# Kernel tuning notes

Measured on AMD Instinct MI355X. Metric: run time of the kernel, lower is better.

The kernel has to match this reference:

```python
import jax, jax.numpy as jnp
import numpy as np
from jax.scipy.special import xlogy

LAMBDA_XM = 0.05
LAMBDA_SEG2D = 1.0
BN_EPS = 1e-5


def setup_inputs() -> dict:
    key = jax.random.key(0)
    ks = jax.random.split(key, 40)
    S, N, Nv, B, Np, M, H, C, MID = 2, 240000, 80000, 2, 120000, 30000, 64, 20, 16
    Nimg = B * M
    f = lambda i, shape, s=0.05: jax.random.normal(ks[i], shape, jnp.float32) * s
    inp = {
        'img_feat': f(0, (S, Nimg, H), 1.0),
        'pts_feat': f(1, (S, Nv, H), 1.0),
        'coors_inv': jax.random.randint(ks[2], (S, N), 0, Nv),
        'labels': jax.random.randint(ks[3], (N,), 0, C),
        'img_label': jax.random.randint(ks[4], (Nimg,), 0, C),
        'p2img_idx': jax.random.randint(ks[5], (B, M), 0, Np),
        # multihead 3d classifiers (per scale): Linear(H,128)-ReLU-Linear(128,C)
        'w3a': f(6, (S, H, 128)), 'b3a': jnp.zeros((S, 128)),
        'w3b': f(7, (S, 128, C)), 'b3b': jnp.zeros((S, C)),
        # multihead fuse classifiers
        'wfa': f(8, (S, H, 128)), 'bfa': jnp.zeros((S, 128)),
        'wfb': f(9, (S, 128, C)), 'bfb': jnp.zeros((S, C)),
        # attention: fc1(H->H//4), fc2(H->H//4), fc3(H//2->2), conv1/conv2 (1x1 -> linear) + BN
        'fc1w': f(10, (S, H, MID)), 'fc1b': jnp.zeros((S, MID)),
        'fc2w': f(11, (S, H, MID)), 'fc2b': jnp.zeros((S, MID)),
        'fc3w': f(12, (S, 2 * MID, 2)), 'fc3b': jnp.zeros((S, 2)),
        'c1w': f(13, (S, H, H)), 'c1b': jnp.zeros((S, H)),
        'bn1g': jnp.ones((S, H)), 'bn1b': jnp.zeros((S, H)),
        'c2w': f(14, (S, H, H)), 'c2b': jnp.zeros((S, H)),
        'bn2g': jnp.ones((S, H)), 'bn2b': jnp.zeros((S, H)),
        # final classifier Linear(S*H,128)-ReLU-Linear(128,C)
        'clw1': f(15, (S * H, 128)), 'clb1': jnp.zeros((128,)),
        'clw2': f(16, (128, C)), 'clb2': jnp.zeros((C,)),
    }
    return inp


def _mlp2(x, w1, b1, w2, b2):
    return jax.nn.relu(x @ w1 + b1) @ w2 + b2


def _ce(logits, lab):
    logp = jax.nn.log_softmax(logits, -1)
    return -jnp.take_along_axis(logp, lab[:, None], axis=1).mean()


def _lovasz(probs, lab):
    # lovasz-softmax over all classes, averaged over present classes
    C = probs.shape[1]
    fg = jax.nn.one_hot(lab, C, dtype=probs.dtype)  # [N,C]
    errors = jnp.abs(fg - probs)

    def per_class(err_c, fg_c):
        order = jnp.argsort(-err_c)
        e = err_c[order]
        f = fg_c[order]
        gts = f.sum()
        inter = gts - jnp.cumsum(f)
        union = gts + jnp.cumsum(1.0 - f)
        jac = 1.0 - inter / union
        jac = jnp.concatenate([jac[:1], jac[1:] - jac[:-1]])
        return jnp.dot(e, jac)

    losses = jax.vmap(per_class)(errors.T, fg.T)  # [C]
    present = (fg.sum(0) > 0).astype(probs.dtype)
    return jnp.sum(losses * present) / jnp.maximum(present.sum(), 1.0)


def _seg_loss(logits, lab):
    return _ce(logits, lab) + _lovasz(jax.nn.softmax(logits, -1), lab)


def _convbn_relu(x, cw, cb, g, b):
    # 1x1 Conv1d == per-point linear; BN (training-mode batch stats over points)
    y = x @ cw + cb
    mu = y.mean(0)
    var = y.var(0)
    return jax.nn.relu((y - mu) * jax.lax.rsqrt(var + BN_EPS) * g + b)


def reference(img_feat, pts_feat, coors_inv, labels, img_label, p2img_idx,
              w3a, b3a, w3b, b3b, wfa, bfa, wfb, bfb,
              fc1w, fc1b, fc2w, fc2b, fc3w, fc3b,
              c1w, c1b, bn1g, bn1b, c2w, c2b, bn2g, bn2b,
              clw1, clb1, clw2, clb2):
    S, Nv, H = pts_feat.shape
    C = w3b.shape[-1]
    B, M = p2img_idx.shape
    N = labels.shape[0]
    Np = N // B
    # p2img_mapping: per-batch gather composed to one global gather (batch blocks are contiguous/equal)
    gidx = (jnp.arange(B)[:, None] * Np + p2img_idx).reshape(-1)  # [Nimg]

    loss = jnp.float32(0.0)
    feats = []
    for s in range(S):
        pred3d = _mlp2(pts_feat[s], w3a[s], b3a[s], w3b[s], b3b[s])  # [Nv,C]
        # voxelize_labels: majority vote per voxel (== unique+scatter_max count argmax)
        counts = jnp.zeros((Nv, C), jnp.float32).at[coors_inv[s], labels].add(1.0)
        vox_lab = jnp.argmax(counts, axis=1)  # [Nv]
        # gather voxel feats/preds to image-projected points (fused gather)
        idx = coors_inv[s][gidx]  # [Nimg]
        p = pts_feat[s][idx]      # [Nimg,H] pseudo feats
        pts_pred = pred3d[idx]    # [Nimg,C]
        v = img_feat[s]           # [Nimg,H] valid (image) feats
        # Attention fusion
        w = jax.nn.sigmoid(
            jnp.concatenate([p @ fc1w[s] + fc1b[s], v @ fc2w[s] + fc2b[s]], -1) @ fc3w[s] + fc3b[s])  # [Nimg,2]
        fuse = (_convbn_relu(p, c1w[s], c1b[s], bn1g[s], bn1b[s]) * w[:, 0:1]
                + _convbn_relu(v, c2w[s], c2b[s], bn2g[s], bn2b[s]) * w[:, 1:2])
        feats.append(fuse)
        fuse_pred = _mlp2(fuse, wfa[s], bfa[s], wfb[s], bfb[s])
        loss = loss + _seg_loss(pred3d, vox_lab)
        loss = loss + _seg_loss(fuse_pred, img_label) * LAMBDA_SEG2D / S
        # F.kl_div(log_softmax(pts_pred), softmax(fuse_pred)), reduction='mean' over all elements
        pf = jax.nn.softmax(fuse_pred, -1)
        kl = jnp.mean(xlogy(pf, pf) - pf * jax.nn.log_softmax(pts_pred, -1))
        loss = loss + kl * LAMBDA_XM / S
    img_logits = _mlp2(jnp.concatenate(feats, -1), clw1, clb1, clw2, clb2)
    loss = loss + _seg_loss(img_logits, img_label)
    return loss
```

## Files before the change

### kernel.cpp

```cpp
#include <hip/hip_runtime.h>
#include <stdint.h>

static constexpr int NV   = 80000;
static constexpr int NPT  = 240000;
static constexpr int NIMG = 60000;
static constexpr int Hh   = 64;
static constexpr int Cc   = 20;
static constexpr int NPp  = 120000;
static constexpr int Mm   = 30000;
static constexpr int NB     = 8192;
static constexpr int NCH    = 16;
static constexpr int NBLK_GA  = (NIMG + 63) / 64;
static constexpr int NBLK_MLP = NV / 64;
static constexpr int NBLK_CNT = (NPT + 255) / 256;
static constexpr int NBLK_FILL_NV = (NV + 255) / 256;
static constexpr int NBLK_FILL_NI = (NIMG + 255) / 256;
static constexpr int NBLK_HIST = Cc * NCH;
#define BN_EPS 1e-5f

using bf16x8 = __attribute__((ext_vector_type(8))) short;
using f32x4  = __attribute__((ext_vector_type(4))) float;

__device__ __forceinline__ float waveReduce(float v) {
  #pragma unroll
  for (int o = 32; o > 0; o >>= 1) v += __shfl_down(v, o);
  return v;
}
__device__ __forceinline__ short f2bf(float f) {
  uint32_t u = __float_as_uint(f);
  return (short)((u + 0x7FFFu + ((u >> 16) & 1u)) >> 16);
}
__device__ __forceinline__ float bf2f(uint32_t h) { return __uint_as_float(h << 16); }
__device__ __forceinline__ uint32_t pk2(float a, float b) {
  return ((uint32_t)(uint16_t)f2bf(a)) | ((uint32_t)(uint16_t)f2bf(b) << 16);
}

struct PackDesc { const float* src; short* dst; int K, Nr, nt; };
struct PackArgs { PackDesc d[14]; };

__global__ void __launch_bounds__(256)
k_pack_zero(PackArgs pa,
            const float* __restrict__ fc1w, const float* __restrict__ fc1b,
            const float* __restrict__ fc2w, const float* __restrict__ fc2b,
            const float* __restrict__ fc3w, const float* __restrict__ fc3b,
            float* __restrict__ attEffs,
            uint4* __restrict__ zb, int zq) {
  if (blockIdx.x >= 128) {
    const uint4 z = make_uint4(0u, 0u, 0u, 0u);
    int i = (blockIdx.x - 128) * 256 + threadIdx.x;
    for (; i < zq; i += 256 * 256) zb[i] = z;
    return;
  }
  const int stride = 128 * 256;
  for (int di = 0; di < 14; di++) {
    const float* src = pa.d[di].src;
    short* dst = pa.d[di].dst;
    int K = pa.d[di].K, Nr = pa.d[di].Nr, ntiles = pa.d[di].nt;
    int total = (K / 32) * ntiles * 512;
    for (int idx = blockIdx.x * blockDim.x + threadIdx.x; idx < total; idx += stride) {
      int j = idx & 7, lane = (idx >> 3) & 63, tile = idx >> 9;
      int nt = tile % ntiles, kt = tile / ntiles;
      int k = kt * 32 + (lane >> 4) * 8 + j;
      int n = nt * 16 + (lane & 15);
      float v = (n < Nr) ? src[(size_t)k * Nr + n] : 0.f;
      dst[idx] = f2bf(v);
    }
  }
  if (blockIdx.x < 2 && threadIdx.x < 64) {
    int s = blockIdx.x, t = threadIdx.x;
    const float* f1w = fc1w + s * 64 * 16; const float* f1b = fc1b + s * 16;
    const float* f2w = fc2w + s * 64 * 16; const float* f2b = fc2b + s * 16;
    const float* f3w = fc3w + s * 64;      const float* f3b = fc3b + s * 2;
    float* aE = attEffs + s * 320;
    float p0 = 0.f, p1 = 0.f, v0 = 0.f, v1 = 0.f;
    #pragma unroll
    for (int j = 0; j < 16; j++) {
      p0 = fmaf(f1w[t * 16 + j], f3w[j * 2], p0);
      p1 = fmaf(f1w[t * 16 + j], f3w[j * 2 + 1], p1);
      v0 = fmaf(f2w[t * 16 + j], f3w[(16 + j) * 2], v0);
      v1 = fmaf(f2w[t * 16 + j], f3w[(16 + j) * 2 + 1], v1);
    }
    aE[t * 2] = p0; aE[t * 2 + 1] = p1;
    aE[128 + t * 2] = v0; aE[128 + t * 2 + 1] = v1;
    if (t == 0) {
      float b0 = f3b[0], b1 = f3b[1];
      for (int j = 0; j < 16; j++) {
        b0 += f1b[j] * f3w[j * 2] + f2b[j] * f3w[(16 + j) * 2];
        b1 += f1b[j] * f3w[j * 2 + 1] + f2b[j] * f3w[(16 + j) * 2 + 1];
      }
      aE[256] = b0; aE[257] = b1;
    }
  }
}

__device__ void scanbin_body(const uint32_t* __restrict__ Hb, const uint32_t* __restrict__ HFb,
                             int n, int call, float* __restrict__ lossesC5,
                             int* __restrict__ gts5, int cls) {
  __shared__ int sWC[4], sWF[4];
  __shared__ float sRedF[4];
  int t = threadIdx.x;
  int lane = t & 63, w = t >> 6;
  const uint32_t* Hc  = Hb  + (size_t)cls * NB;
  const uint32_t* HFc = HFb + (size_t)cls * NB;
  int locC = 0, locF = 0;
  #pragma unroll
  for (int i = 0; i < 8; i++) {
    uint4 cv = *(const uint4*)(Hc  + t * 32 + i * 4);
    uint4 fv = *(const uint4*)(HFc + t * 32 + i * 4);
    locC += (int)(cv.x + cv.y + cv.z + cv.w);
    locF += (int)(fv.x + fv.y + fv.z + fv.w);
  }
  int sc = locC, sf = locF;
  #pragma unroll
  for (int o = 1; o < 64; o <<= 1) {
    int a = __shfl_up(sc, o);
    int b = __shfl_up(sf, o);
    if (lane >= o) { sc += a; sf += b; }
  }
  if (lane == 63) { sWC[w] = sc; sWF[w] = sf; }
  __syncthreads();
  int offC = 0, offF = 0, Ftot = 0;
  #pragma unroll
  for (int ww = 0; ww < 4; ww++) {
    int fc = sWF[ww];
    Ftot += fc;
    if (ww < w) { offC += sWC[ww]; offF += fc; }
  }
  int runC = offC + sc - locC;
  int runF = offF + sf - locF;
  float gts = (float)Ftot;
  float contrib = 0.f;
  #pragma unroll
  for (int i = 0; i < 8; i++) {
    uint4 cv = *(const uint4*)(Hc  + t * 32 + i * 4);
    uint4 fv = *(const uint4*)(HFc + t * 32 + i * 4);
    uint32_t ca[4] = {cv.x, cv.y, cv.z, cv.w};
    uint32_t fa[4] = {fv.x, fv.y, fv.z, fv.w};
    #pragma unroll
    for (int j = 0; j < 4; j++) {
      int cnt = (int)ca[j], fgc = (int)fa[j];
      runC += cnt; runF += fgc;
      if (cnt > 0 && Ftot > 0) {
        float r0 = (float)(n - runC);
        float F0 = (float)(Ftot - runF);
        float r1 = r0 + (float)cnt;
        float F1 = F0 + (float)fgc;
        float emean = __uint_as_float((uint32_t)(t * 32 + i * 4 + j) << 17);
        contrib += emean * (r1 / (gts + r1 - F1) - r0 / (gts + r0 - F0));
      }
    }
  }
  contrib = waveReduce(contrib);
// ... 15 lines not shown
  constexpr int KT1 = D / 32;
  const int t = threadIdx.x;
  const int lane = t & 63, w = t >> 6;
  const int m = lane & 15, quad = lane >> 4;
  const int rowA = 16 * w + m;
  bf16x8 a1[KT1];
  #pragma unroll
  for (int kt = 0; kt < KT1; kt++)
    a1[kt] = *(const bf16x8*)(sXb + rowA * LDB + kt * 32 + quad * 8);
  const bf16x8* b1 = (const bf16x8*)pw1;
  #pragma unroll
  for (int nt = 0; nt < 8; nt++) {
    f32x4 c = {0.f, 0.f, 0.f, 0.f};
    #pragma unroll
    for (int kt = 0; kt < KT1; kt++)
      c = __builtin_amdgcn_mfma_f32_16x16x32_bf16(a1[kt], b1[(kt * 8 + nt) * 64 + lane], c, 0, 0, 0);
    int col = nt * 16 + m;
    float bc = B1[col];
    #pragma unroll
    for (int reg = 0; reg < 4; reg++)
      sH[(16 * w + quad * 4 + reg) * 136 + col] = f2bf(fmaxf(c[reg] + bc, 0.f));
  }
  __syncthreads();
  bf16x8 a2[4];
  #pragma unroll
  for (int kt = 0; kt < 4; kt++)
    a2[kt] = *(const bf16x8*)(sH + rowA * 136 + kt * 32 + quad * 8);
  const bf16x8* b2 = (const bf16x8*)pw2;
  #pragma unroll
  for (int nt = 0; nt < 2; nt++) {
    f32x4 c = {0.f, 0.f, 0.f, 0.f};
    #pragma unroll
    for (int kt = 0; kt < 4; kt++)
      c = __builtin_amdgcn_mfma_f32_16x16x32_bf16(a2[kt], b2[(kt * 2 + nt) * 64 + lane], c, 0, 0, 0);
    int col = nt * 16 + m;
    if (col < Cc) {
      float bc = B2[col];
      #pragma unroll
      for (int reg = 0; reg < 4; reg++) {
        int gr = r0 + 16 * w + quad * 4 + reg;
        if (gr < rows) Out[(size_t)gr * Cc + col] = c[reg] + bc;
      }
    }
  }
}

__device__ void mlp64_body(int bid0, const float* __restrict__ X,
    const short* __restrict__ pw1, const float* __restrict__ B1,
    const short* __restrict__ pw2, const float* __restrict__ B2,
    float* __restrict__ Out, int rows, char* smem) {
  short* sXb = (short*)smem;
  short* sH  = (short*)(smem + 9216);
  int t = threadIdx.x, r0 = bid0 * 64;
  for (int i = t; i < 1024; i += 256) {
    int r = i >> 4, k4 = (i & 15) * 4;
    int gr = r0 + r;
    float4 v = (gr < rows) ? *(const float4*)(X + (size_t)gr * 64 + k4)
                           : make_float4(0.f, 0.f, 0.f, 0.f);
    uint2 p; p.x = pk2(v.x, v.y); p.y = pk2(v.z, v.w);
    *(uint2*)(sXb + r * 72 + k4) = p;
  }
  __syncthreads();
  mfma_mlp_body<64>(sXb, sH, r0, rows, pw1, B1, pw2, B2, Out);
}

__device__ void mlp128_body(int bid0, const uint16_t* __restrict__ Xh,
    const short* __restrict__ pw1, const float* __restrict__ B1,
    const short* __restrict__ pw2, const float* __restrict__ B2,
    float* __restrict__ Out, char* smem) {
  short* sXb = (short*)smem;
  short* sH  = (short*)(smem + 17408);
  int t = threadIdx.x, r0 = bid0 * 64;
  for (int i = t; i < 2048; i += 256) {
    int r = i >> 5, k4 = (i & 31) * 4;
    int gr = r0 + r;
    uint2 p = (gr < NIMG) ? *(const uint2*)(Xh + (size_t)gr * 128 + k4) : make_uint2(0u, 0u);
    *(uint2*)(sXb + r * 136 + k4) = p;
  }
  __syncthreads();
  mfma_mlp_body<128>(sXb, sH, r0, NIMG, pw1, B1, pw2, B2, Out);
}

__device__ void cnt_body(int bid0, const int* __restrict__ ci, const int* __restrict__ labels,
                         int* __restrict__ counts, const int* __restrict__ p2img,
                         int* __restrict__ idx) {
  int i = bid0 * 256 + threadIdx.x;
  if (i < NIMG) {
    int b = (i >= Mm) ? 1 : 0;
    idx[i] = ci[b * NPp + p2img[i]];
  }
  if (i < NPT) atomicAdd(&counts[(size_t)ci[i] * Cc + labels[i]], 1);
}

__device__ void colred_body(int bid0, const float* __restrict__ partials,
                            float* __restrict__ red64) {
  int t = threadIdx.x, j = bid0;
  float v = 0.f;
  for (int b = j; b < NBLK_GA; b += 64) v += partials[(size_t)b * 256 + t];
  red64[j * 256 + t] = v;
}

__device__ void fill_body(int bid0, const float* __restrict__ logits,
                          const int* __restrict__ lab, const int* __restrict__ vcnt,
                          int n, uint16_t* __restrict__ E,
                          float ceScale, float* __restrict__ lossAcc,
                          const float* __restrict__ pred3d, const int* __restrict__ idxg,
                          float klScale) {
  int i = bid0 * 256 + threadIdx.x;
  float total = 0.f;
  if (i < n) {
    int lb;
    if (vcnt) {
      const int* crow = vcnt + (size_t)i * Cc;
      int best = crow[0], arg = 0;
      #pragma unroll
      for (int k = 1; k < Cc; k++) {
        int ck = crow[k];
        if (ck > best) { best = ck; arg = k; }
      }
      lb = arg;
    } else {
      lb = lab[i];
    }
    const float* l = logits + (size_t)i * Cc;
    float m = l[0];
    #pragma unroll
    for (int c = 1; c < Cc; c++) m = fmaxf(m, l[c]);
    float ex[Cc]; float se = 0.f;
    #pragma unroll
    for (int c = 0; c < Cc; c++) { ex[c] = expf(l[c] - m); se += ex[c]; }
    float inv = 1.f / se;
    float lse = logf(se);
    total = -(l[lb] - m - lse) * ceScale;
    #pragma unroll
    for (int c = 0; c < Cc; c++) {
      float prob = ex[c] * inv;
      int fg = (c == lb) ? 1 : 0;
      float err = fg ? (1.f - prob) : prob;
      err = fmaxf(err, 0.f);
      uint32_t key = __float_as_uint(err) >> 17;
      E[(size_t)c * n + i] = (uint16_t)((key << 1) | (uint32_t)fg);
    }
    if (pred3d) {
      const float* q = pred3d + (size_t)idxg[i] * Cc;
      float mq = q[0];
      #pragma unroll
      for (int c = 1; c < Cc; c++) mq = fmaxf(mq, q[c]);
      float sq = 0.f;
      #pragma unroll
      for (int c = 0; c < Cc; c++) sq += expf(q[c] - mq);
      float lsq = logf(sq);
      float kl = 0.f;
      #pragma unroll
      for (int c = 0; c < Cc; c++) {
        float lf = l[c] - m - lse;
        float pf = ex[c] * inv;
        float lq = q[c] - mq - lsq;
        kl += pf * (lf - lq);
      }
      total += kl * klScale;
    }
  }
  total = waveReduce(total);
  __shared__ float sh[4];
  int lane = threadIdx.x & 63, w = threadIdx.x >> 6;
  if (lane == 0) sh[w] = total;
  __syncthreads();
  if (threadIdx.x == 0) atomicAdd(lossAcc, sh[0] + sh[1] + sh[2] + sh[3]);
}

__device__ void hist_body(int bid0, const uint16_t* __restrict__ E, int n,
                          uint32_t* __restrict__ H, uint32_t* __restrict__ HF, char* smem) {
  uint32_t* lcf = (uint32_t*)smem;
// ... 122 lines not shown
  }
  __syncthreads();
  {
    int kind = t >> 6, col = t & 63;
    int nt = col >> 4, mm = col & 15;
    float v = 0.f;
    #pragma unroll
    for (int ww = 0; ww < 4; ww++)
      v += sStat[(ww * 4 + nt) * 64 + kind * 16 + mm];
    partials[(size_t)bid0 * 256 + kind * 64 + col] = v;
  }
  if (t < 64) {
    int gr = r0 + t;
    if (gr < NIMG) {
      float l0 = attEff[256] + sAtt[t * 8] + sAtt[t * 8 + 2] + sAtt[t * 8 + 4] + sAtt[t * 8 + 6];
      float l1 = attEff[257] + sAtt[t * 8 + 1] + sAtt[t * 8 + 3] + sAtt[t * 8 + 5] + sAtt[t * 8 + 7];
      attw[gr * 2]     = 1.f / (1.f + expf(-l0));
      attw[gr * 2 + 1] = 1.f / (1.f + expf(-l1));
    }
  }
}

__device__ void fusemlp_body(int bid0,
    const uint16_t* __restrict__ y1, const uint16_t* __restrict__ y2,
    const float* __restrict__ attw, const float* __restrict__ red64,
    const float* __restrict__ g1, const float* __restrict__ be1,
    const float* __restrict__ g2, const float* __restrict__ be2,
    uint16_t* __restrict__ feats, int s64,
    const short* __restrict__ pw1, const float* __restrict__ B1,
    const short* __restrict__ pw2, const float* __restrict__ B2,
    float* __restrict__ Out, char* smem) {
  short* sXb = (short*)smem;
  short* sH  = (short*)(smem + 9216);
  float* sBn = (float*)(smem + 9216 + 17408);
  int t = threadIdx.x, r0 = bid0 * 64;
  float acc = 0.f;
  #pragma unroll 8
  for (int b = 0; b < 64; b++) acc += red64[b * 256 + t];
  float* sSum = (float*)sH;
  sSum[t] = acc;
  __syncthreads();
  if (t < 64) {
    float nn = (float)NIMG;
    float mu1 = sSum[t] / nn;
    float var1 = sSum[64 + t] / nn - mu1 * mu1;
    float a1 = g1[t] / sqrtf(var1 + BN_EPS);
    sBn[t] = a1; sBn[64 + t] = be1[t] - mu1 * a1;
    float mu2 = sSum[128 + t] / nn;
    float var2 = sSum[192 + t] / nn - mu2 * mu2;
    float a2 = g2[t] / sqrtf(var2 + BN_EPS);
    sBn[128 + t] = a2; sBn[192 + t] = be2[t] - mu2 * a2;
  }
  __syncthreads();
  for (int i = t; i < 1024; i += 256) {
    int r = i >> 4, q = i & 15;
    int gr = r0 + r;
    uint2 zp = make_uint2(0u, 0u);
    if (gr < NIMG) {
      float4 a1 = *(const float4*)(sBn + q * 4);
      float4 c1 = *(const float4*)(sBn + 64 + q * 4);
      float4 a2 = *(const float4*)(sBn + 128 + q * 4);
      float4 c2 = *(const float4*)(sBn + 192 + q * 4);
      uint2 u1 = *(const uint2*)(y1 + (size_t)gr * 64 + q * 4);
      uint2 u2 = *(const uint2*)(y2 + (size_t)gr * 64 + q * 4);
      float w0 = attw[gr * 2], w1 = attw[gr * 2 + 1];
      float zx = fmaxf(fmaf(bf2f(u1.x & 0xffff), a1.x, c1.x), 0.f) * w0
               + fmaxf(fmaf(bf2f(u2.x & 0xffff), a2.x, c2.x), 0.f) * w1;
      float zy = fmaxf(fmaf(bf2f(u1.x >> 16),   a1.y, c1.y), 0.f) * w0
               + fmaxf(fmaf(bf2f(u2.x >> 16),   a2.y, c2.y), 0.f) * w1;
      float zz = fmaxf(fmaf(bf2f(u1.y & 0xffff), a1.z, c1.z), 0.f) * w0
               + fmaxf(fmaf(bf2f(u2.y & 0xffff), a2.z, c2.z), 0.f) * w1;
      float zw = fmaxf(fmaf(bf2f(u1.y >> 16),   a1.w, c1.w), 0.f) * w0
               + fmaxf(fmaf(bf2f(u2.y >> 16),   a2.w, c2.w), 0.f) * w1;
      zp.x = pk2(zx, zy); zp.y = pk2(zz, zw);
      *(uint2*)(feats + (size_t)gr * 128 + s64 + q * 4) = zp;
    }
    *(uint2*)(sXb + r * 72 + q * 4) = zp;
  }
  __syncthreads();
  mfma_mlp_body<64>(sXb, sH, r0, NIMG, pw1, B1, pw2, B2, Out);
}

__global__ void __launch_bounds__(256)
k_start2(const float* __restrict__ X0, const float* __restrict__ X1,
         const short* pw1_0, const float* B1_0, const short* pw2_0, const float* B2_0, float* out0,
         const short* pw1_1, const float* B1_1, const short* pw2_1, const float* B2_1, float* out1,
         const int* __restrict__ ci0, const int* __restrict__ ci1,
         const int* __restrict__ labels, const int* __restrict__ p2img,
         int* __restrict__ counts0, int* __restrict__ counts1,
         int* __restrict__ idx0, int* __restrict__ idx1) {
  __shared__ char smem[26624];
  int bid = blockIdx.x;
  if (bid < NBLK_MLP) { mlp64_body(bid, X0, pw1_0, B1_0, pw2_0, B2_0, out0, NV, smem); return; }
  bid -= NBLK_MLP;
  if (bid < NBLK_MLP) { mlp64_body(bid, X1, pw1_1, B1_1, pw2_1, B2_1, out1, NV, smem); return; }
  bid -= NBLK_MLP;
  if (bid < NBLK_CNT) { cnt_body(bid, ci0, labels, counts0, p2img, idx0); return; }
  cnt_body(bid - NBLK_CNT, ci1, labels, counts1, p2img, idx1);
}

__global__ void __launch_bounds__(256)
k_fill2(const float* __restrict__ l0, const int* __restrict__ vc0, uint16_t* __restrict__ E0,
        const float* __restrict__ l1, const int* __restrict__ vc1, uint16_t* __restrict__ E1,
        float ce, float* __restrict__ lossAcc) {
  if (blockIdx.x < NBLK_FILL_NV)
    fill_body(blockIdx.x, l0, nullptr, vc0, NV, E0, ce, lossAcc, nullptr, nullptr, 0.f);
  else
    fill_body(blockIdx.x - NBLK_FILL_NV, l1, nullptr, vc1, NV, E1, ce, lossAcc, nullptr, nullptr, 0.f);
}

__global__ void __launch_bounds__(256)
k_hist2x(const uint16_t* __restrict__ E0, uint32_t* H0, uint32_t* HF0,
         const uint16_t* __restrict__ E1, uint32_t* H1, uint32_t* HF1, int n) {
  __shared__ char smem[32768];
  if (blockIdx.x < NBLK_HIST) hist_body(blockIdx.x, E0, n, H0, HF0, smem);
  else hist_body(blockIdx.x - NBLK_HIST, E1, n, H1, HF1, smem);
}

__global__ void __launch_bounds__(256)
k_gattx(const float* __restrict__ pts, const int* __restrict__ idx, const float* __restrict__ img,
        const short* pc1, const float* c1b, const short* pc2, const float* c2b,
        const float* attEff, uint16_t* y1, uint16_t* y2, float* attw, float* partials,
        const uint32_t* Ha, const uint32_t* HFa, int na, int calla,
        const uint32_t* Hb, const uint32_t* HFb, int nb, int callb,
        int nscan,
        const float* crPart, float* crRed,
        float* lossesC5, int* gts5) {
  __shared__ char smem[24576];
  int bid = blockIdx.x;
  if (bid < nscan * Cc) {
    if (bid < Cc) scanbin_body(Ha, HFa, na, calla, lossesC5, gts5, bid);
    else scanbin_body(Hb, HFb, nb, callb, lossesC5, gts5, bid - Cc);
    return;
  }
  bid -= nscan * Cc;
  if (crPart) {
    if (bid < 64) { colred_body(bid, crPart, crRed); return; }
    bid -= 64;
  }
  gatt_body(bid, pts, idx, img, pc1, c1b, pc2, c2b, attEff, y1, y2, attw, partials, smem);
}

__global__ void __launch_bounds__(256)
k_fusex(const uint16_t* y1, const uint16_t* y2, const float* attw, const float* red64,
        const float* g1, const float* be1, const float* g2, const float* be2,
        uint16_t* feats, int s64,
        const short* pw1, const float* B1, const short* pw2, const float* B2, float* Out,
        const float* crPart, float* crRed,
        const float* fl_logits, const int* fl_lab, uint16_t* fl_E, float fl_ce,
        const float* fl_pred, const int* fl_idx, float fl_kl, float* lossAcc) {
  __shared__ char smem[27648];
  int bid = blockIdx.x;
  if (bid < NBLK_GA) {
    fusemlp_body(bid, y1, y2, attw, red64, g1, be1, g2, be2, feats, s64,
                 pw1, B1, pw2, B2, Out, smem);
    return;
  }
  bid -= NBLK_GA;
  if (crPart) { colred_body(bid, crPart, crRed); return; }
  fill_body(bid, fl_logits, fl_lab, nullptr, NIMG, fl_E, fl_ce, lossAcc, fl_pred, fl_idx, fl_kl);
}

__global__ void __launch_bounds__(256)
k_fill_hist(const float* __restrict__ l, const int* __restrict__ lab, uint16_t* Ew, float ce,
            const float* __restrict__ pred, const int* __restrict__ idxg, float kl,
            float* lossAcc,
            const uint16_t* __restrict__ Er, int nh, uint32_t* H, uint32_t* HF) {
  __shared__ char smem[32768];
  if (blockIdx.x < NBLK_FILL_NI)
    fill_body(blockIdx.x, l, lab, nullptr, NIMG, Ew, ce, lossAcc, pred, idxg, kl);
  else
    hist_body(blockIdx.x - NBLK_FILL_NI, Er, nh, H, HF, smem);
}

__global__ void __launch_bounds__(256)
k_finx(const uint16_t* __restrict__ Xh,
       const short* pw1, const float* B1, const short* pw2, const float* B2, float* Out,
       const uint16_t* __restrict__ Er, int nh, uint32_t* Hr, uint32_t* HFr,
       const uint32_t* Hs, const uint32_t* HFs, int ns, int calls,
       float* lossesC5, int* gts5) {
  __shared__ char smem[34816];
  int bid = blockIdx.x;
  if (bid < NBLK_GA) { mlp128_body(bid, Xh, pw1, B1, pw2, B2, Out, smem); return; }
  bid -= NBLK_GA;
  if (bid < NBLK_HIST) { hist_body(bid, Er, nh, Hr, HFr, smem); return; }
  scanbin_body(Hs, HFs, ns, calls, lossesC5, gts5, bid - NBLK_HIST);
}

__global__ void __launch_bounds__(256)
k_fill_scan(const float* __restrict__ l, const int* __restrict__ lab, uint16_t* Ew, float ce,
            float* lossAcc,
            const uint32_t* Hs, const uint32_t* HFs, int ns, int calls,
            float* lossesC5, int* gts5) {
  if (blockIdx.x < NBLK_FILL_NI)
    fill_body(blockIdx.x, l, lab, nullptr, NIMG, Ew, ce, lossAcc, nullptr, nullptr, 0.f);
  else
    scanbin_body(Hs, HFs, ns, calls, lossesC5, gts5, blockIdx.x - NBLK_FILL_NI);
}

__global__ void __launch_bounds__(256)
k_hist1(const uint16_t* __restrict__ E, int n, uint32_t* H, uint32_t* HF) {
  __shared__ char smem[32768];
  hist_body(blockIdx.x, E, n, H, HF, smem);
}

__global__ void __launch_bounds__(256)
k_scanbin5(const uint32_t* Hb, const uint32_t* HFb, int n, int call,
           float* lossesC5, int* gts5) {
  scanbin_body(Hb, HFb, n, call, lossesC5, gts5, blockIdx.x);
}

__global__ void k_final(const float* __restrict__ lossAcc,
                        const float* __restrict__ lossesC5, const int* __restrict__ gts5,
                        float* __restrict__ out) {
  const float coefs[5] = {1.0f, 0.5f, 1.0f, 0.5f, 1.0f};
  float loss = lossAcc[0];
  for (int call = 0; call < 5; call++) {
    float s = 0.f; int np = 0;
    for (int c = 0; c < Cc; c++)
      if (gts5[call * 32 + c] > 0) { s += lossesC5[call * 32 + c]; np++; }
    loss += coefs[call] * s / (float)(np > 0 ? np : 1);
  }
  out[0] = loss;
}

extern "C" void kernel_launch(void* const* d_in, const int* in_sizes, int n_in,
                              void* d_out, int out_size, void* d_ws, size_t ws_size,
                              hipStream_t stream) {
  const float* img_feat = (const float*)d_in[0];
  const float* pts_feat = (const float*)d_in[1];
  const int* coors_inv  = (const int*)d_in[2];
  const int* labels     = (const int*)d_in[3];
  const int* img_label  = (const int*)d_in[4];
  const int* p2img      = (const int*)d_in[5];
  const float* w3a = (const float*)d_in[6];
  const float* b3a = (const float*)d_in[7];
  const float* w3b = (const float*)d_in[8];
  const float* b3b = (const float*)d_in[9];
  const float* wfa = (const float*)d_in[10];
  const float* bfa = (const float*)d_in[11];
  const float* wfb = (const float*)d_in[12];
  const float* bfb = (const float*)d_in[13];
  const float* fc1w = (const float*)d_in[14];
  const float* fc1b = (const float*)d_in[15];
  const float* fc2w = (const float*)d_in[16];
  const float* fc2b = (const float*)d_in[17];
  const float* fc3w = (const float*)d_in[18];
  const float* fc3b = (const float*)d_in[19];
  const float* c1w  = (const float*)d_in[20];
  const float* c1b  = (const float*)d_in[21];
  const float* bn1g = (const float*)d_in[22];
  const float* bn1b = (const float*)d_in[23];
  const float* c2w  = (const float*)d_in[24];
  const float* c2b  = (const float*)d_in[25];
  const float* bn2g = (const float*)d_in[26];
  const float* bn2b = (const float*)d_in[27];
  const float* clw1 = (const float*)d_in[28];
  const float* clb1 = (const float*)d_in[29];
  const float* clw2 = (const float*)d_in[30];
  const float* clb2 = (const float*)d_in[31];
  (void)in_sizes; (void)n_in; (void)out_size; (void)ws_size;

  char* ws = (char*)d_ws;
  size_t off = 0;
  auto alloc = [&](size_t bytes) { void* p = ws + off; off += (bytes + 255) & ~(size_t)255; return p; };
  uint16_t* feats = (uint16_t*)alloc((size_t)NIMG * 128 * 2);
  float* pred3d0 = (float*)alloc((size_t)NV * Cc * 4);
  float* pred3d1 = (float*)alloc((size_t)NV * Cc * 4);
  int* idx0 = (int*)alloc((size_t)NIMG * 4);
  int* idx1 = (int*)alloc((size_t)NIMG * 4);
  uint16_t* y1a = (uint16_t*)alloc((size_t)NIMG * Hh * 2);
  uint16_t* y2a = (uint16_t*)alloc((size_t)NIMG * Hh * 2);
  uint16_t* y1b = (uint16_t*)alloc((size_t)NIMG * Hh * 2);
  uint16_t* y2b = (uint16_t*)alloc((size_t)NIMG * Hh * 2);
  uint16_t* E0 = (uint16_t*)alloc((size_t)Cc * NV * 2);
  uint16_t* E1 = (uint16_t*)alloc((size_t)Cc * NV * 2);
  float* partials0 = (float*)alloc((size_t)NBLK_GA * 256 * 4);
  float* partials1 = (float*)alloc((size_t)NBLK_GA * 256 * 4);
  float* red64_0 = (float*)alloc(64 * 256 * 4);
  float* red64_1 = (float*)alloc(64 * 256 * 4);
  float* attw0 = (float*)alloc((size_t)NIMG * 2 * 4);
  float* attw1 = (float*)alloc((size_t)NIMG * 2 * 4);
  float* fusepred0 = (float*)alloc((size_t)NIMG * Cc * 4);
  float* fusepred1 = (float*)alloc((size_t)NIMG * Cc * 4);
  short* pwAll = (short*)alloc(86016 * 2);
  short* pw3a0 = pwAll,          * pw3a1 = pwAll + 8192;
  short* pwfa0 = pwAll + 16384,  * pwfa1 = pwAll + 24576;
  short* pw3b0 = pwAll + 32768,  * pw3b1 = pwAll + 36864;
  short* pwfb0 = pwAll + 40960,  * pwfb1 = pwAll + 45056;
  short* pcl1  = pwAll + 49152;
  short* pcl2  = pwAll + 65536;
  short* pc1w0 = pwAll + 69632,  * pc1w1 = pwAll + 73728;
  short* pc2w0 = pwAll + 77824,  * pc2w1 = pwAll + 81920;
  float* attEffs = (float*)alloc(2 * 320 * 4);
  size_t zsize = 1024 + (size_t)5 * 2 * Cc * NB * 4 + (size_t)2 * NV * Cc * 4;
  char* zbase = (char*)alloc(zsize);
  float* lossAcc  = (float*)zbase;
  float* lossesC5 = (float*)zbase + 32;
  int*   gts5     = (int*)((float*)zbase + 192);
  uint32_t* Hbase = (uint32_t*)(zbase + 1024);
  auto Hc  = [&](int call) { return Hbase + (size_t)call * 2 * Cc * NB; };
  auto HFc = [&](int call) { return Hbase + (size_t)call * 2 * Cc * NB + (size_t)Cc * NB; };
  int* counts0 = (int*)(zbase + 1024 + (size_t)5 * 2 * Cc * NB * 4);
  int* counts1 = counts0 + (size_t)NV * Cc;
  int zq = (int)(zsize / 16);

  const float kl = 0.025f / ((float)NIMG * Cc);
  const float* pf0 = pts_feat;
  const float* pf1 = pts_feat + (size_t)NV * Hh;
  const float* if0 = img_feat;
  const float* if1 = img_feat + (size_t)NIMG * Hh;
  const int* ci0 = coors_inv;
  const int* ci1 = coors_inv + NPT;

  PackArgs pa;
  pa.d[0]  = {w3a,        pw3a0, 64, 128, 8};
  pa.d[1]  = {w3a + 8192, pw3a1, 64, 128, 8};
  pa.d[2]  = {wfa,        pwfa0, 64, 128, 8};
  pa.d[3]  = {wfa + 8192, pwfa1, 64, 128, 8};
  pa.d[4]  = {w3b,        pw3b0, 128, 20, 2};
  pa.d[5]  = {w3b + 2560, pw3b1, 128, 20, 2};
  pa.d[6]  = {wfb,        pwfb0, 128, 20, 2};
  pa.d[7]  = {wfb + 2560, pwfb1, 128, 20, 2};
  pa.d[8]  = {clw1,       pcl1, 128, 128, 8};
  pa.d[9]  = {clw2,       pcl2, 128, 20, 2};
  pa.d[10] = {c1w,        pc1w0, 64, 64, 4};
  pa.d[11] = {c1w + 4096, pc1w1, 64, 64, 4};
  pa.d[12] = {c2w,        pc2w0, 64, 64, 4};
  pa.d[13] = {c2w + 4096, pc2w1, 64, 64, 4};
  k_pack_zero<<<128 + 256, 256, 0, stream>>>(pa, fc1w, fc1b, fc2w, fc2b, fc3w, fc3b,
                                             attEffs, (uint4*)zbase, zq);

  k_start2<<<2 * NBLK_MLP + 2 * NBLK_CNT, 256, 0, stream>>>(
      pf0, pf1,
      pw3a0, b3a, pw3b0, b3b, pred3d0,
      pw3a1, b3a + 128, pw3b1, b3b + Cc, pred3d1,
      ci0, ci1, labels, p2img, counts0, counts1, idx0, idx1);

  k_fill2<<<2 * NBLK_FILL_NV, 256, 0, stream>>>(pred3d0, counts0, E0,
                                                pred3d1, counts1, E1,
                                                1.0f / NV, lossAcc);

  k_hist2x<<<2 * NBLK_HIST, 256, 0, stream>>>(E0, Hc(0), HFc(0), E1, Hc(2), HFc(2), NV);

  k_gattx<<<2 * Cc + NBLK_GA, 256, 0, stream>>>(
      pf0, idx0, if0, pc1w0, c1b, pc2w0, c2b, attEffs,
      y1a, y2a, attw0, partials0,
      Hc(0), HFc(0), NV, 0, Hc(2), HFc(2), NV, 2, 2,
      nullptr, nullptr, lossesC5, gts5);

  k_gattx<<<64 + NBLK_GA, 256, 0, stream>>>(
      pf1, idx1, if1, pc1w1, c1b + 64, pc2w1, c2b + 64, attEffs + 320,
      y1b, y2b, attw1, partials1,
      nullptr, nullptr, 0, 0, nullptr, nullptr, 0, 0, 0,
      partials0, red64_0, lossesC5, gts5);

  k_fusex<<<NBLK_GA + 64, 256, 0, stream>>>(
      y1a, y2a, attw0, red64_0, bn1g, bn1b, bn2g, bn2b, feats, 0,
      pwfa0, bfa, pwfb0, bfb, fusepred0,
      partials1, red64_1,
      nullptr, nullptr, nullptr, 0.f, nullptr, nullptr, 0.f, lossAcc);

  k_fusex<<<NBLK_GA + NBLK_FILL_NI, 256, 0, stream>>>(
      y1b, y2b, attw1, red64_1, bn1g + 64, bn1b + 64, bn2g + 64, bn2b + 64, feats, 64,
      pwfa1, bfa + 128, pwfb1, bfb + Cc, fusepred1,
      nullptr, nullptr,
      fusepred0, img_label, E0, 0.5f / NIMG, pred3d0, idx0, kl, lossAcc);

  k_fill_hist<<<NBLK_FILL_NI + NBLK_HIST, 256, 0, stream>>>(
      fusepred1, img_label, E1, 0.5f / NIMG, pred3d1, idx1, kl, lossAcc,
      E0, NIMG, Hc(1), HFc(1));

  k_finx<<<NBLK_GA + NBLK_HIST + Cc, 256, 0, stream>>>(
      feats, pcl1, clb1, pcl2, clb2, fusepred0,
      E1, NIMG, Hc(3), HFc(3),
      Hc(1), HFc(1), NIMG, 1, lossesC5, gts5);

  k_fill_scan<<<NBLK_FILL_NI + Cc, 256, 0, stream>>>(
      fusepred0, img_label, E0, 1.0f / NIMG, lossAcc,
      Hc(3), HFc(3), NIMG, 3, lossesC5, gts5);

  k_hist1<<<NBLK_HIST, 256, 0, stream>>>(E0, NIMG, Hc(4), HFc(4));

  k_scanbin5<<<Cc, 256, 0, stream>>>(Hc(4), HFc(4), NIMG, 4, lossesC5, gts5);

  k_final<<<1, 1, 0, stream>>>(lossAcc, lossesC5, gts5, (float*)d_out);
}
```

Before: 350.4 us.

## Restructure kernel schedule to merge independent stages into fewer launches

Moves the image-index gather into the pack/zero kernel so both scales' gated-attention bodies can run together with the 3D MLPs and count atomics in one kernel. Colred is merged with the voxel fills, both fuse MLPs with the voxel histograms, and the image fills with the final classifier and scans. The final classifier output goes to a new buffer and error array (finalpred, E2), so the two image fills and the final fill no longer serialize through reused buffers. This cuts the launch count from about 12 to 8 and gives the GPU more independent work per launch, at the cost of extra memory and a larger per-kernel shared-memory footprint.

Measured after the change: 347.1 us. No clear change (-1.0%).

```diff
diff --git a/kernel.cpp b/kernel.cpp
--- a/kernel.cpp
+++ b/kernel.cpp
@@ -16,6 +16,7 @@
 static constexpr int NBLK_FILL_NV = (NV + 255) / 256;
 static constexpr int NBLK_FILL_NI = (NIMG + 255) / 256;
 static constexpr int NBLK_HIST = Cc * NCH;
+static constexpr int NBLK_IDX  = (NIMG + 255) / 256;
 #define BN_EPS 1e-5f
 
 using bf16x8 = __attribute__((ext_vector_type(8))) short;
@@ -44,10 +45,25 @@
             const float* __restrict__ fc2w, const float* __restrict__ fc2b,
             const float* __restrict__ fc3w, const float* __restrict__ fc3b,
             float* __restrict__ attEffs,
-            uint4* __restrict__ zb, int zq) {
-  if (blockIdx.x >= 128) {
+            uint4* __restrict__ zb, int zq,
+            const int* __restrict__ ci0, const int* __restrict__ ci1,
+            const int* __restrict__ p2img,
+            int* __restrict__ idx0, int* __restrict__ idx1) {
+  int bid = blockIdx.x;
+  if (bid >= 384) {
+    bid -= 384;
+    if (bid < NBLK_IDX) {
+      int i = bid * 256 + threadIdx.x;
+      if (i < NIMG) idx0[i] = ci0[(i >= Mm ? NPp : 0) + p2img[i]];
+    } else {
+      int i = (bid - NBLK_IDX) * 256 + threadIdx.x;
+      if (i < NIMG) idx1[i] = ci1[(i >= Mm ? NPp : 0) + p2img[i]];
+    }
+    return;
+  }
+  if (bid >= 128) {
     const uint4 z = make_uint4(0u, 0u, 0u, 0u);
-    int i = (blockIdx.x - 128) * 256 + threadIdx.x;
+    int i = (bid - 128) * 256 + threadIdx.x;
     for (; i < zq; i += 256 * 256) zb[i] = z;
     return;
   }
@@ -57,7 +73,7 @@
     short* dst = pa.d[di].dst;
     int K = pa.d[di].K, Nr = pa.d[di].Nr, ntiles = pa.d[di].nt;
     int total = (K / 32) * ntiles * 512;
-    for (int idx = blockIdx.x * blockDim.x + threadIdx.x; idx < total; idx += stride) {
+    for (int idx = bid * 256 + threadIdx.x; idx < total; idx += stride) {
       int j = idx & 7, lane = (idx >> 3) & 63, tile = idx >> 9;
       int nt = tile % ntiles, kt = tile / ntiles;
       int k = kt * 32 + (lane >> 4) * 8 + j;
@@ -66,8 +82,8 @@
       dst[idx] = f2bf(v);
     }
   }
-  if (blockIdx.x < 2 && threadIdx.x < 64) {
-    int s = blockIdx.x, t = threadIdx.x;
+  if (bid < 2 && threadIdx.x < 64) {
+    int s = bid, t = threadIdx.x;
     const float* f1w = fc1w + s * 64 * 16; const float* f1b = fc1b + s * 16;
     const float* f2w = fc2w + s * 64 * 16; const float* f2b = fc2b + s * 16;
     const float* f3w = fc3w + s * 64;      const float* f3b = fc3b + s * 2;
@@ -249,13 +265,8 @@
 }
 
 __device__ void cnt_body(int bid0, const int* __restrict__ ci, const int* __restrict__ labels,
-                         int* __restrict__ counts, const int* __restrict__ p2img,
-                         int* __restrict__ idx) {
+                         int* __restrict__ counts) {
   int i = bid0 * 256 + threadIdx.x;
-  if (i < NIMG) {
-    int b = (i >= Mm) ? 1 : 0;
-    idx[i] = ci[b * NPp + p2img[i]];
-  }
   if (i < NPT) atomicAdd(&counts[(size_t)ci[i] * Cc + labels[i]], 1);
 }
 
@@ -544,126 +555,143 @@
 }
 
 __global__ void __launch_bounds__(256)
-k_start2(const float* __restrict__ X0, const float* __restrict__ X1,
-         const short* pw1_0, const float* B1_0, const short* pw2_0, const float* B2_0, float* out0,
-         const short* pw1_1, const float* B1_1, const short* pw2_1, const float* B2_1, float* out1,
-         const int* __restrict__ ci0, const int* __restrict__ ci1,
-         const int* __restrict__ labels, const int* __restrict__ p2img,
-         int* __restrict__ counts0, int* __restrict__ counts1,
-         int* __restrict__ idx0, int* __restrict__ idx1) {
+k_mega2(const float* __restrict__ pf0, const float* __restrict__ pf1,
+        const int* __restrict__ idx0, const int* __restrict__ idx1,
+        const float* __restrict__ if0, const float* __restrict__ if1,
+        const short* pc1w0, const short* pc1w1, const short* pc2w0, const short* pc2w1,
+        const float* c1b, const float* c2b, const float* attEffs,
+        uint16_t* y1a, uint16_t* y2a, uint16_t* y1b, uint16_t* y2b,
+        float* attw0, float* attw1, float* partials0, float* partials1,
+        const short* pw3a0, const float* b3a, const short* pw3b0, const float* b3b,
+        const short* pw3a1, const short* pw3b1,
+        float* pred3d0, float* pred3d1,
+        const int* __restrict__ ci0, const int* __restrict__ ci1,
+        const int* __restrict__ labels,
+        int* __restrict__ counts0, int* __restrict__ counts1) {
   __shared__ char smem[26624];
   int bid = blockIdx.x;
-  if (bid < NBLK_MLP) { mlp64_body(bid, X0, pw1_0, B1_0, pw2_0, B2_0, out0, NV, smem); return; }
+  if (bid < NBLK_GA) {
+    gatt_body(bid, pf0, idx0, if0, pc1w0, c1b, pc2w0, c2b, attEffs,
+              y1a, y2a, attw0, partials0, smem);
+    return;
+  }
+  bid -= NBLK_GA;
+  if (bid < NBLK_GA) {
+    gatt_body(bid, pf1, idx1, if1, pc1w1, c1b + 64, pc2w1, c2b + 64, attEffs + 320,
+              y1b, y2b, attw1, partials1, smem);
+    return;
+  }
+  bid -= NBLK_GA;
+  if (bid < NBLK_MLP) { mlp64_body(bid, pf0, pw3a0, b3a, pw3b0, b3b, pred3d0, NV, smem); return; }
   bid -= NBLK_MLP;
-  if (bid < NBLK_MLP) { mlp64_body(bid, X1, pw1_1, B1_1, pw2_1, B2_1, out1, NV, smem); return; }
+  if (bid < NBLK_MLP) { mlp64_body(bid, pf1, pw3a1, b3a + 128, pw3b1, b3b + Cc, pred3d1, NV, smem); return; }
   bid -= NBLK_MLP;
-  if (bid < NBLK_CNT) { cnt_body(bid, ci0, labels, counts0, p2img, idx0); return; }
-  cnt_body(bid - NBLK_CNT, ci1, labels, counts1, p2img, idx1);
+  if (bid < NBLK_CNT) { cnt_body(bid, ci0, labels, counts0); return; }
+  cnt_body(bid - NBLK_CNT, ci1, labels, counts1);
 }
 
 __global__ void __launch_bounds__(256)
-k_fill2(const float* __restrict__ l0, const int* __restrict__ vc0, uint16_t* __restrict__ E0,
-        const float* __restrict__ l1, const int* __restrict__ vc1, uint16_t* __restrict__ E1,
-        float ce, float* __restrict__ lossAcc) {
-  if (blockIdx.x < NBLK_FILL_NV)
-    fill_body(blockIdx.x, l0, nullptr, vc0, NV, E0, ce, lossAcc, nullptr, nullptr, 0.f);
-  else
-    fill_body(blockIdx.x - NBLK_FILL_NV, l1, nullptr, vc1, NV, E1, ce, lossAcc, nullptr, nullptr, 0.f);
+k_fill_colred(const float* __restrict__ l0, const int* __restrict__ vc0, uint16_t* __restrict__ E0,
+              const float* __restrict__ l1, const int* __restrict__ vc1, uint16_t* __restrict__ E1,
+              float ce, float* __restrict__ lossAcc,
+              const float* partials0, float* red64_0,
+              const float* partials1, float* red64_1) {
+  int bid = blockIdx.x;
+  if (bid < NBLK_FILL_NV) {
+    fill_body(bid, l0, nullptr, vc0, NV, E0, ce, lossAcc, nullptr, nullptr, 0.f);
+    return;
+  }
+  bid -= NBLK_FILL_NV;
+  if (bid < NBLK_FILL_NV) {
+    fill_body(bid, l1, nullptr, vc1, NV, E1, ce, lossAcc, nullptr, nullptr, 0.f);
+    return;
+  }
+  bid -= NBLK_FILL_NV;
+  if (bid < 64) { colred_body(bid, partials0, red64_0); return; }
+  colred_body(bid - 64, partials1, red64_1);
 }
 
 __global__ void __launch_bounds__(256)
-k_hist2x(const uint16_t* __restrict__ E0, uint32_t* H0, uint32_t* HF0,
-         const uint16_t* __restrict__ E1, uint32_t* H1, uint32_t* HF1, int n) {
+k_fuse2_hist2(const uint16_t* y1a, const uint16_t* y2a, const float* attw0, const float* red64_0,
+              const uint16_t* y1b, const uint16_t* y2b, const float* attw1, const float* red64_1,
+              const float* bn1g, const float* bn1b, const float* bn2g, const float* bn2b,
+              uint16_t* feats,
+              const short* pwfa0, const float* bfa, const short* pwfb0, const float* bfb,
+              const short* pwfa1, const short* pwfb1,
+              float* fusepred0, float* fusepred1,
+              const uint16_t* __restrict__ E0, uint32_t* H0, uint32_t* HF0,
+              const uint16_t* __restrict__ E1, uint32_t* H2, uint32_t* HF2) {
   __shared__ char smem[32768];
-  if (blockIdx.x < NBLK_HIST) hist_body(blockIdx.x, E0, n, H0, HF0, smem);
-  else hist_body(blockIdx.x - NBLK_HIST, E1, n, H1, HF1, smem);
-}
-
-__global__ void __launch_bounds__(256)
-k_gattx(const float* __restrict__ pts, const int* __restrict__ idx, const float* __restrict__ img,
-        const short* pc1, const float* c1b, const short* pc2, const float* c2b,
-        const float* attEff, uint16_t* y1, uint16_t* y2, float* attw, float* partials,
-        const uint32_t* Ha, const uint32_t* HFa, int na, int calla,
-        const uint32_t* Hb, const uint32_t* HFb, int nb, int callb,
-        int nscan,
-        const float* crPart, float* crRed,
-        float* lossesC5, int* gts5) {
-  __shared__ char smem[24576];
-  int bid = blockIdx.x;
-  if (bid < nscan * Cc) {
-    if (bid < Cc) scanbin_body(Ha, HFa, na, calla, lossesC5, gts5, bid);
-    else scanbin_body(Hb, HFb, nb, callb, lossesC5, gts5, bid - Cc);
-    return;
-  }
-  bid -= nscan * Cc;
-  if (crPart) {
-    if (bid < 64) { colred_body(bid, crPart, crRed); return; }
-    bid -= 64;
-  }
-  gatt_body(bid, pts, idx, img, pc1, c1b, pc2, c2b, attEff, y1, y2, attw, partials, smem);
-}
-
-__global__ void __launch_bounds__(256)
-k_fusex(const uint16_t* y1, const uint16_t* y2, const float* attw, const float* red64,
-        const float* g1, const float* be1, const float* g2, const float* be2,
-        uint16_t* feats, int s64,
-        const short* pw1, const float* B1, const short* pw2, const float* B2, float* Out,
-        const float* crPart, float* crRed,
-        const float* fl_logits, const int* fl_lab, uint16_t* fl_E, float fl_ce,
-        const float* fl_pred, const int* fl_idx, float fl_kl, float* lossAcc) {
-  __shared__ char smem[27648];
   int bid = blockIdx.x;
   if (bid < NBLK_GA) {
-    fusemlp_body(bid, y1, y2, attw, red64, g1, be1, g2, be2, feats, s64,
-                 pw1, B1, pw2, B2, Out, smem);
+    fusemlp_body(bid, y1a, y2a, attw0, red64_0, bn1g, bn1b, bn2g, bn2b, feats, 0,
+                 pwfa0, bfa, pwfb0, bfb, fusepred0, smem);
     return;
   }
   bid -= NBLK_GA;
-  if (crPart) { colred_body(bid, crPart, crRed); return; }
-  fill_body(bid, fl_logits, fl_lab, nullptr, NIMG, fl_E, fl_ce, lossAcc, fl_pred, fl_idx, fl_kl);
+  if (bid < NBLK_GA) {
+    fusemlp_body(bid, y1b, y2b, attw1, red64_1, bn1g + 64, bn1b + 64, bn2g + 64, bn2b + 64,
+                 feats, 64, pwfa1, bfa + 128, pwfb1, bfb + Cc, fusepred1, smem);
+    return;
+  }
+  bid -= NBLK_GA;
+  if (bid < NBLK_HIST) { hist_body(bid, E0, NV, H0, HF0, smem); return; }
+  hist_body(bid - NBLK_HIST, E1, NV, H2, HF2, smem);
 }
 
 __global__ void __launch_bounds__(256)
-k_fill_hist(const float* __restrict__ l, const int* __restrict__ lab, uint16_t* Ew, float ce,
-            const float* __restrict__ pred, const int* __restrict__ idxg, float kl,
-            float* lossAcc,
-            const uint16_t* __restrict__ Er, int nh, uint32_t* H, uint32_t* HF) {
-  __shared__ char smem[32768];
-  if (blockIdx.x < NBLK_FILL_NI)
-    fill_body(blockIdx.x, l, lab, nullptr, NIMG, Ew, ce, lossAcc, pred, idxg, kl);
-  else
-    hist_body(blockIdx.x - NBLK_FILL_NI, Er, nh, H, HF, smem);
-}
-
-__global__ void __launch_bounds__(256)
-k_finx(const uint16_t* __restrict__ Xh,
-       const short* pw1, const float* B1, const short* pw2, const float* B2, float* Out,
-       const uint16_t* __restrict__ Er, int nh, uint32_t* Hr, uint32_t* HFr,
-       const uint32_t* Hs, const uint32_t* HFs, int ns, int calls,
-       float* lossesC5, int* gts5) {
+k_finx2(const uint16_t* __restrict__ feats,
+        const short* pcl1, const float* clb1, const short* pcl2, const float* clb2,
+        float* finalpred,
+        const float* fusepred0, const float* pred3d0, const int* idx0, uint16_t* E0w,
+        const float* fusepred1, const float* pred3d1, const int* idx1, uint16_t* E1w,
+        const int* __restrict__ img_label, float ce, float kl, float* lossAcc,
+        const uint32_t* H0, const uint32_t* HF0,
+        const uint32_t* H2, const uint32_t* HF2,
+        float* lossesC5, int* gts5) {
   __shared__ char smem[34816];
   int bid = blockIdx.x;
-  if (bid < NBLK_GA) { mlp128_body(bid, Xh, pw1, B1, pw2, B2, Out, smem); return; }
+  if (bid < NBLK_GA) { mlp128_body(bid, feats, pcl1, clb1, pcl2, clb2, finalpred, smem); return; }
   bid -= NBLK_GA;
-  if (bid < NBLK_HIST) { hist_body(bid, Er, nh, Hr, HFr, smem); return; }
-  scanbin_body(Hs, HFs, ns, calls, lossesC5, gts5, bid - NBLK_HIST);
+  if (bid < NBLK_FILL_NI) {
+    fill_body(bid, fusepred0, img_label, nullptr, NIMG, E0w, ce, lossAcc, pred3d0, idx0, kl);
+    return;
+  }
+  bid -= NBLK_FILL_NI;
+  if (bid < NBLK_FILL_NI) {
+    fill_body(bid, fusepred1, img_label, nullptr, NIMG, E1w, ce, lossAcc, pred3d1, idx1, kl);
+    return;
+  }
+  bid -= NBLK_FILL_NI;
+  if (bid < Cc) { scanbin_body(H0, HF0, NV, 0, lossesC5, gts5, bid); return; }
+  scanbin_body(H2, HF2, NV, 2, lossesC5, gts5, bid - Cc);
 }
 
 __global__ void __launch_bounds__(256)
-k_fill_scan(const float* __restrict__ l, const int* __restrict__ lab, uint16_t* Ew, float ce,
-            float* lossAcc,
-            const uint32_t* Hs, const uint32_t* HFs, int ns, int calls,
-            float* lossesC5, int* gts5) {
-  if (blockIdx.x < NBLK_FILL_NI)
-    fill_body(blockIdx.x, l, lab, nullptr, NIMG, Ew, ce, lossAcc, nullptr, nullptr, 0.f);
-  else
-    scanbin_body(Hs, HFs, ns, calls, lossesC5, gts5, blockIdx.x - NBLK_FILL_NI);
+k_hist2_fill(const uint16_t* __restrict__ E0, uint32_t* H1, uint32_t* HF1,
+             const uint16_t* __restrict__ E1, uint32_t* H3, uint32_t* HF3,
+             const float* __restrict__ finalpred, const int* __restrict__ img_label,
+             uint16_t* __restrict__ E2, float ce, float* lossAcc) {
+  __shared__ char smem[32768];
+  int bid = blockIdx.x;
+  if (bid < NBLK_HIST) { hist_body(bid, E0, NIMG, H1, HF1, smem); return; }
+  bid -= NBLK_HIST;
+  if (bid < NBLK_HIST) { hist_body(bid, E1, NIMG, H3, HF3, smem); return; }
+  fill_body(bid - NBLK_HIST, finalpred, img_label, nullptr, NIMG, E2, ce, lossAcc,
+            nullptr, nullptr, 0.f);
 }
 
 __global__ void __launch_bounds__(256)
-k_hist1(const uint16_t* __restrict__ E, int n, uint32_t* H, uint32_t* HF) {
+k_hist_scan2(const uint16_t* __restrict__ E2, uint32_t* H4, uint32_t* HF4,
+             const uint32_t* H1, const uint32_t* HF1,
+             const uint32_t* H3, const uint32_t* HF3,
+             float* lossesC5, int* gts5) {
   __shared__ char smem[32768];
-  hist_body(blockIdx.x, E, n, H, HF, smem);
+  int bid = blockIdx.x;
+  if (bid < NBLK_HIST) { hist_body(bid, E2, NIMG, H4, HF4, smem); return; }
+  bid -= NBLK_HIST;
+  if (bid < Cc) { scanbin_body(H1, HF1, NIMG, 1, lossesC5, gts5, bid); return; }
+  scanbin_body(H3, HF3, NIMG, 3, lossesC5, gts5, bid - Cc);
 }
 
 __global__ void __launch_bounds__(256)
@@ -737,6 +765,7 @@
   uint16_t* y2b = (uint16_t*)alloc((size_t)NIMG * Hh * 2);
   uint16_t* E0 = (uint16_t*)alloc((size_t)Cc * NV * 2);
   uint16_t* E1 = (uint16_t*)alloc((size_t)Cc * NV * 2);
+  uint16_t* E2 = (uint16_t*)alloc((size_t)Cc * NIMG * 2);
   float* partials0 = (float*)alloc((size_t)NBLK_GA * 256 * 4);
   float* partials1 = (float*)alloc((size_t)NBLK_GA * 256 * 4);
   float* red64_0 = (float*)alloc(64 * 256 * 4);
@@ -745,6 +774,7 @@
   float* attw1 = (float*)alloc((size_t)NIMG * 2 * 4);
   float* fusepred0 = (float*)alloc((size_t)NIMG * Cc * 4);
   float* fusepred1 = (float*)alloc((size_t)NIMG * Cc * 4);
+  float* finalpred = (float*)alloc((size_t)NIMG * Cc * 4);
   short* pwAll = (short*)alloc(86016 * 2);
   short* pw3a0 = pwAll,          * pw3a1 = pwAll + 8192;
   short* pwfa0 = pwAll + 16384,  * pwfa1 = pwAll + 24576;
@@ -790,59 +820,40 @@
   pa.d[11] = {c1w + 4096, pc1w1, 64, 64, 4};
   pa.d[12] = {c2w,        pc2w0, 64, 64, 4};
   pa.d[13] = {c2w + 4096, pc2w1, 64, 64, 4};
-  k_pack_zero<<<128 + 256, 256, 0, stream>>>(pa, fc1w, fc1b, fc2w, fc2b, fc3w, fc3b,
-                                             attEffs, (uint4*)zbase, zq);
-
-  k_start2<<<2 * NBLK_MLP + 2 * NBLK_CNT, 256, 0, stream>>>(
-      pf0, pf1,
-      pw3a0, b3a, pw3b0, b3b, pred3d0,
-      pw3a1, b3a + 128, pw3b1, b3b + Cc, pred3d1,
-      ci0, ci1, labels, p2img, counts0, counts1, idx0, idx1);
-
-  k_fill2<<<2 * NBLK_FILL_NV, 256, 0, stream>>>(pred3d0, counts0, E0,
-                                                pred3d1, counts1, E1,
-                                                1.0f / NV, lossAcc);
-
-  k_hist2x<<<2 * NBLK_HIST, 256, 0, stream>>>(E0, Hc(0), HFc(0), E1, Hc(2), HFc(2), NV);
-
-  k_gattx<<<2 * Cc + NBLK_GA, 256, 0, stream>>>(
-      pf0, idx0, if0, pc1w0, c1b, pc2w0, c2b, attEffs,
-      y1a, y2a, attw0, partials0,
-      Hc(0), HFc(0), NV, 0, Hc(2), HFc(2), NV, 2, 2,
-      nullptr, nullptr, lossesC5, gts5);
-
-  k_gattx<<<64 + NBLK_GA, 256, 0, stream>>>(
-      pf1, idx1, if1, pc1w1, c1b + 64, pc2w1, c2b + 64, attEffs + 320,
-      y1b, y2b, attw1, partials1,
-      nullptr, nullptr, 0, 0, nullptr, nullptr, 0, 0, 0,
-      partials0, red64_0, lossesC5, gts5);
-
-  k_fusex<<<NBLK_GA + 64, 256, 0, stream>>>(
-      y1a, y2a, attw0, red64_0, bn1g, bn1b, bn2g, bn2b, feats, 0,
-      pwfa0, bfa, pwfb0, bfb, fusepred0,
-      partials1, red64_1,
-      nullptr, nullptr, nullptr, 0.f, nullptr, nullptr, 0.f, lossAcc);
-
-  k_fusex<<<NBLK_GA + NBLK_FILL_NI, 256, 0, stream>>>(
-      y1b, y2b, attw1, red64_1, bn1g + 64, bn1b + 64, bn2g + 64, bn2b + 64, feats, 64,
-      pwfa1, bfa + 128, pwfb1, bfb + Cc, fusepred1,
-      nullptr, nullptr,
-      fusepred0, img_label, E0, 0.5f / NIMG, pred3d0, idx0, kl, lossAcc);
-
-  k_fill_hist<<<NBLK_FILL_NI + NBLK_HIST, 256, 0, stream>>>(
-      fusepred1, img_label, E1, 0.5f / NIMG, pred3d1, idx1, kl, lossAcc,
-      E0, NIMG, Hc(1), HFc(1));
-
-  k_finx<<<NBLK_GA + NBLK_HIST + Cc, 256, 0, stream>>>(
-      feats, pcl1, clb1, pcl2, clb2, fusepred0,
-      E1, NIMG, Hc(3), HFc(3),
-      Hc(1), HFc(1), NIMG, 1, lossesC5, gts5);
-
-  k_fill_scan<<<NBLK_FILL_NI + Cc, 256, 0, stream>>>(
-      fusepred0, img_label, E0, 1.0f / NIMG, lossAcc,
-      Hc(3), HFc(3), NIMG, 3, lossesC5, gts5);
-
-  k_hist1<<<NBLK_HIST, 256, 0, stream>>>(E0, NIMG, Hc(4), HFc(4));
+  k_pack_zero<<<384 + 2 * NBLK_IDX, 256, 0, stream>>>(
+      pa, fc1w, fc1b, fc2w, fc2b, fc3w, fc3b, attEffs,
+      (uint4*)zbase, zq, ci0, ci1, p2img, idx0, idx1);
+
+  k_mega2<<<2 * NBLK_GA + 2 * NBLK_MLP + 2 * NBLK_CNT, 256, 0, stream>>>(
+      pf0, pf1, idx0, idx1, if0, if1,
+      pc1w0, pc1w1, pc2w0, pc2w1, c1b, c2b, attEffs,
+      y1a, y2a, y1b, y2b, attw0, attw1, partials0, partials1,
+      pw3a0, b3a, pw3b0, b3b, pw3a1, pw3b1, pred3d0, pred3d1,
+      ci0, ci1, labels, counts0, counts1);
+
+  k_fill_colred<<<2 * NBLK_FILL_NV + 128, 256, 0, stream>>>(
+      pred3d0, counts0, E0, pred3d1, counts1, E1, 1.0f / NV, lossAcc,
+      partials0, red64_0, partials1, red64_1);
+
+  k_fuse2_hist2<<<2 * NBLK_GA + 2 * NBLK_HIST, 256, 0, stream>>>(
+      y1a, y2a, attw0, red64_0, y1b, y2b, attw1, red64_1,
+      bn1g, bn1b, bn2g, bn2b, feats,
+      pwfa0, bfa, pwfb0, bfb, pwfa1, pwfb1, fusepred0, fusepred1,
+      E0, Hc(0), HFc(0), E1, Hc(2), HFc(2));
+
+  k_finx2<<<NBLK_GA + 2 * NBLK_FILL_NI + 2 * Cc, 256, 0, stream>>>(
+      feats, pcl1, clb1, pcl2, clb2, finalpred,
+      fusepred0, pred3d0, idx0, E0,
+      fusepred1, pred3d1, idx1, E1,
+      img_label, 0.5f / NIMG, kl, lossAcc,
+      Hc(0), HFc(0), Hc(2), HFc(2), lossesC5, gts5);
+
+  k_hist2_fill<<<2 * NBLK_HIST + NBLK_FILL_NI, 256, 0, stream>>>(
+      E0, Hc(1), HFc(1), E1, Hc(3), HFc(3),
+      finalpred, img_label, E2, 1.0f / NIMG, lossAcc);
+
+  k_hist_scan2<<<NBLK_HIST + 2 * Cc, 256, 0, stream>>>(
+      E2, Hc(4), HFc(4), Hc(1), HFc(1), Hc(3), HFc(3), lossesC5, gts5);
 
   k_scanbin5<<<Cc, 256, 0, stream>>>(Hc(4), HFc(4), NIMG, 4, lossesC5, gts5);
 
```
